# Kernel optimization log

Hardware: AMD Instinct MI355X
Metric: run time of the kernel (lower is better)

## Reference

```python
import jax, jax.numpy as jnp
import numpy as np

RANGES = {"measure": 256, "beat": 16, "position": 128, "duration": 128, "pitch": 256,
          "instrument": 129, "velocity": 128, "key_sign": 24, "time_sign": 48, "tempo": 49}
R_TOTAL = sum(RANGES.values())  # 1162
NUMERATORS = jnp.array([1, 2, 3, 4, 5, 6, 7, 8, 9, 10, 12, 16], dtype=jnp.int32)
TOT_NUM = 12
NEG = jnp.float32(-1e9)


def _prefix_gather(x, axis=1):
    # value at position i becomes the cumulative value at index min(i+1, S-1):
    # reproduces the tf mask `range(S) <= idx+1` (prefix up to i+1 inclusive).
    S = x.shape[axis]
    idx = jnp.minimum(jnp.arange(S) + 1, S - 1)
    return jnp.take(x, idx, axis=axis)


def _present_mask(song, dtype_id, feat, R):
    # occ[b,i,v] = True iff some token j<=i+1 has type dtype_id and song[b,j,feat]==v
    # (vectorized form of tensor_scatter_nd_max over a prefix, via one-hot + cummax)
    match = song[..., 0] == dtype_id                       # [B,S]
    onehot = (song[..., feat][..., None] == jnp.arange(R)) & match[..., None]
    cum = jax.lax.cummax(onehot.astype(jnp.int32), axis=1)
    return _prefix_gather(cum, 1).astype(bool)             # [B,S,R]


def _has_any(song, dtype_id):
    match = (song[..., 0] == dtype_id).astype(jnp.int32)
    return _prefix_gather(jax.lax.cummax(match, axis=1), 1).astype(bool)  # [B,S]


def _last_value(song, dtype_id, feat):
    # song[b, argmax_j(match*j) , feat] over the prefix j<=i+1; tf argmax of all
    # zeros returns 0, reproduced by where(match, j, 0) + cummax.
    match = song[..., 0] == dtype_id
    j = jnp.arange(song.shape[1])
    last_idx = _prefix_gather(jax.lax.cummax(jnp.where(match, j, 0), axis=1), 1)
    return jnp.take_along_axis(song[..., feat], last_idx, axis=1)  # [B,S]


def _forward(song, chosen_type, scores):
    B, S, _ = song.shape
    Rm, Rb = RANGES["measure"], RANGES["beat"]
    ar_m = jnp.arange(RANGES["measure"]); ar_b = jnp.arange(RANGES["beat"])
    ar_p = jnp.arange(RANGES["position"])
    ar_ks = jnp.arange(RANGES["key_sign"]); ar_ts = jnp.arange(RANGES["time_sign"])
    ar_tp = jnp.arange(RANGES["tempo"])
    t = chosen_type[..., None]  # [B,S,1]

    inst_present = _present_mask(song, 1, 6, RANGES["instrument"])  # [B,S,129]
    has_inst = inst_present.any(-1, keepdims=True)

    last_ks = _last_value(song, 4, 8);  oh_ks = last_ks[..., None] == ar_ks
    last_ts = _last_value(song, 5, 9);  oh_ts = last_ts[..., None] == ar_ts
    last_tp = _last_value(song, 6, 10); oh_tp = last_tp[..., None] == ar_tp
    has_ks = _has_any(song, 4)[..., None]
    has_ts = _has_any(song, 5)[..., None]

    # ---- chosen_type == 3 (note-like token) ----
    min_measure = song[..., 1]
    pred_m = jnp.argmax(scores[..., :Rm], axis=-1).astype(jnp.int32)
    c1 = pred_m == min_measure
    min_beat = jnp.where(c1, song[..., 2], 0)
    pred_b = jnp.argmax(scores[..., Rm:Rm + Rb], axis=-1).astype(jnp.int32)
    c2 = c1 & (pred_b == min_beat)
    min_pos = jnp.where(c2, song[..., 3], 0)
    max_beat = NUMERATORS[jnp.mod(last_ts, TOT_NUM)]  # get_max_beat_from_time_sign
    m3 = ar_m >= min_measure[..., None]
    b3 = (ar_b >= min_beat[..., None]) & (ar_b < max_beat[..., None])
    p3 = ar_p >= min_pos[..., None]

    # ---- chosen_type == 1 (instrument): forbid already-present instruments ----
    inst1 = jnp.where(has_inst, ~inst_present, True)

    # ---- chosen_type in 4..6 (key_sign / time_sign / tempo) ----
    min_m46 = jnp.where((song[..., 2] == 0) & (song[..., 3] == 0),
                        song[..., 1], song[..., 1] + 1)
    m46 = ar_m >= min_m46[..., None]
    ks4 = jnp.where(has_ks, ~oh_ks, True)
    ts5 = jnp.where(has_ts, ~oh_ts, True)
    tp6 = ~oh_tp

    is3 = t == 3
    measure_mask = jnp.where(is3, m3, jnp.where((t >= 4) & (t <= 6), m46, True))
    beat_mask = jnp.where(is3, b3, True)
    position_mask = jnp.where(is3, p3, True)
    duration_mask = jnp.ones((B, S, RANGES["duration"]), bool)
    pitch_mask = jnp.ones((B, S, RANGES["pitch"]), bool)
    instrument_mask = jnp.where(is3, inst_present, jnp.where(t == 1, inst1, True))
    velocity_mask = jnp.ones((B, S, RANGES["velocity"]), bool)
    key_sign_mask = jnp.where(is3, oh_ks, jnp.where(t == 4, ks4, True))
    time_sign_mask = jnp.where(is3, oh_ts, jnp.where(t == 5, ts5, True))
    tempo_mask = jnp.where(is3, oh_tp, jnp.where(t == 6, tp6, True))

    mask = jnp.concatenate([measure_mask, beat_mask, position_mask, duration_mask,
                            pitch_mask, instrument_mask, velocity_mask,
                            key_sign_mask, time_sign_mask, tempo_mask], axis=-1)
    return jnp.where(mask, scores, NEG)  # masked logits [B,S,R_TOTAL]


def setup_inputs() -> dict:
    key = jax.random.key(0)
    k_song, k_type, k_scores = jax.random.split(key, 3)
    B, S = 8, 2047  # SEQ_LEN-1 with SEQ_LEN=2048
    col_max = [8, RANGES["measure"], RANGES["beat"], RANGES["position"],
               RANGES["duration"], RANGES["pitch"], RANGES["instrument"],
               RANGES["velocity"], RANGES["key_sign"], RANGES["time_sign"],
               RANGES["tempo"]]
    kcols = jax.random.split(k_song, 11)
    song = jnp.stack([jax.random.randint(kcols[c], (B, S), 0, col_max[c],
                                         dtype=jnp.int32) for c in range(11)], axis=-1)
    chosen_type = jax.random.randint(k_type, (B, S), 0, 8, dtype=jnp.int32)
    scores = jax.random.normal(k_scores, (B, S, R_TOTAL), dtype=jnp.float32)
    return {"song": song, "chosen_type": chosen_type, "scores": scores}


def reference(song, chosen_type, scores):
    return _forward(song, chosen_type, scores)
```

## Files before the change

kernel.cpp:

```cpp
#include <hip/hip_runtime.h>
#include <cstdint>
#include <cstddef>

#define S_LEN 2047
#define BATCH 8
#define R_TOT 1162
#define NCHUNK 8
#define NEGV (-1e9f)

#define CARRY_OFF 393024

__device__ __constant__ int d_numerators[12] = {1, 2, 3, 4, 5, 6, 7, 8, 9, 10, 12, 16};

__global__ __launch_bounds__(256) void scan_local(const int* __restrict__ song,
                                                  unsigned* __restrict__ local) {
    const int b = blockIdx.x >> 3;
    const int c = blockIdx.x & 7;
    const int tid = threadIdx.x;
    const int j = c * 256 + tid;
    __shared__ unsigned lds_f[3][256];
    __shared__ unsigned lds_inst[5][256];
    const unsigned HAS = 1u << 16;
    const long base = (long)b * S_LEN;

    unsigned e_f[3] = {0, 0, 0};
    unsigned e_inst[5] = {0, 0, 0, 0, 0};
    if (j < S_LEN) {
        const int* rj = song + (base + j) * 11;
        const int type = rj[0];
        if (type == 4)      e_f[0] = HAS | (unsigned)rj[8];
        else if (type == 5) e_f[1] = HAS | (unsigned)rj[9];
        else if (type == 6) e_f[2] = HAS | (unsigned)rj[10];
        else if (type == 1) { const int v = rj[6]; e_inst[v >> 5] = 1u << (v & 31); }
    }
#pragma unroll
    for (int w = 0; w < 3; w++) lds_f[w][tid] = e_f[w];
#pragma unroll
    for (int w = 0; w < 5; w++) lds_inst[w][tid] = e_inst[w];
    __syncthreads();

    for (int off = 1; off < 256; off <<= 1) {
        unsigned p_f[3] = {0, 0, 0};
        unsigned p_inst[5] = {0, 0, 0, 0, 0};
        if (tid >= off) {
#pragma unroll
            for (int w = 0; w < 3; w++) p_f[w] = lds_f[w][tid - off];
#pragma unroll
            for (int w = 0; w < 5; w++) p_inst[w] = lds_inst[w][tid - off];
        }
        __syncthreads();
        if (tid >= off) {
#pragma unroll
            for (int w = 0; w < 3; w++) {
                if (!(e_f[w] & HAS)) e_f[w] = p_f[w];
                lds_f[w][tid] = e_f[w];
            }
#pragma unroll
            for (int w = 0; w < 5; w++) {
                e_inst[w] |= p_inst[w];
                lds_inst[w][tid] = e_inst[w];
            }
        }
        __syncthreads();
    }

    if (j < S_LEN) {
        const unsigned w0 =
            (e_f[0] & 0xFFu) | ((e_f[1] & 0xFFu) << 8) | ((e_f[2] & 0xFFu) << 16) |
            (((e_f[0] >> 16) & 1u) << 24) | (((e_f[1] >> 16) & 1u) << 25) |
            (((e_f[2] >> 16) & 1u) << 26);
        unsigned* sp = local + (size_t)(base + j) * 6;
        sp[0] = w0;
#pragma unroll
        for (int w = 0; w < 5; w++) sp[1 + w] = e_inst[w];
    }
}

__global__ __launch_bounds__(64) void scan_carry(const int* __restrict__ song,
                                                 const unsigned* __restrict__ local,
                                                 unsigned* __restrict__ carry) {
    const int b = threadIdx.x;
    if (b >= BATCH) return;
    const int* r0 = song + (size_t)b * S_LEN * 11;
    unsigned cks = (unsigned)r0[8], cts = (unsigned)r0[9], ctp = (unsigned)r0[10];
    unsigned chas = 0;
    unsigned cinst[5] = {0, 0, 0, 0, 0};
    for (int c = 0; c < NCHUNK; c++) {
        unsigned* cp = carry + ((size_t)b * NCHUNK + c) * 6;
        cp[0] = (cks & 0xFFu) | ((cts & 0xFFu) << 8) | ((ctp & 0xFFu) << 16) | (chas << 24);
#pragma unroll
        for (int w = 0; w < 5; w++) cp[1 + w] = cinst[w];
        const int pos = min((c + 1) * 256, S_LEN) - 1;
        const unsigned* lp = local + ((size_t)b * S_LEN + pos) * 6;
        const unsigned a0 = lp[0];
        if ((a0 >> 24) & 1u) cks = a0 & 0xFFu;
        if ((a0 >> 25) & 1u) cts = (a0 >> 8) & 0xFFu;
        if ((a0 >> 26) & 1u) ctp = (a0 >> 16) & 0xFFu;
        chas |= (a0 >> 24) & 7u;
#pragma unroll
        for (int w = 0; w < 5; w++) cinst[w] |= lp[1 + w];
    }
}

__global__ __launch_bounds__(256) void mask_kernel(const int* __restrict__ song,
                                                   const int* __restrict__ ctype,
                                                   const float* __restrict__ scores,
                                                   const unsigned* __restrict__ local,
                                                   const unsigned* __restrict__ carry,
                                                   float* __restrict__ out) {
    const int row = blockIdx.x;
    const int tid = threadIdx.x;
    const int b = row / S_LEN;
    const int i = row - b * S_LEN;

    __shared__ float s_val[128];
    __shared__ int   s_idx[128];
    __shared__ float sb_val[8];
    __shared__ int   sb_idx[8];
    __shared__ int   s_info[10];
    __shared__ int   f_info[17];

    const size_t rbase = (size_t)row * R_TOT;
    const float2* s2 = (const float2*)(scores + rbase);
    float2* o2 = (float2*)(out + rbase);

    const float2 r0 = s2[tid];
    const float2 r1 = s2[tid + 256];
    float2 r2 = make_float2(0.f, 0.f);
    if (tid < 69) r2 = s2[tid + 512];

    if (tid < 128) {
        const bool sec = (r0.y > r0.x);
        s_val[tid] = sec ? r0.y : r0.x;
        s_idx[tid] = 2 * tid + (sec ? 1 : 0);
    } else if (tid < 136) {
        const bool sec = (r0.y > r0.x);
        sb_val[tid - 128] = sec ? r0.y : r0.x;
        sb_idx[tid - 128] = (2 * tid - 256) + (sec ? 1 : 0);
    } else if (tid < 142) {
        const int w = tid - 136;
        const int e = min(i + 1, S_LEN - 1);
        const unsigned lw = local[((size_t)b * S_LEN + e) * 6 + w];
        const unsigned cw = carry[((size_t)b * NCHUNK + (e >> 8)) * 6 + w];
        unsigned v;
        if (w == 0) {
            const unsigned ks = ((lw >> 24) & 1u) ? (lw & 0xFFu) : (cw & 0xFFu);
            const unsigned ts = ((lw >> 25) & 1u) ? ((lw >> 8) & 0xFFu) : ((cw >> 8) & 0xFFu);
            const unsigned tp = ((lw >> 26) & 1u) ? ((lw >> 16) & 0xFFu) : ((cw >> 16) & 0xFFu);
            const unsigned hks = ((lw >> 24) | (cw >> 24)) & 1u;
            const unsigned hts = ((lw >> 25) | (cw >> 25)) & 1u;
            v = ks | (ts << 8) | (tp << 16) | (hks << 24) | (hts << 25);
        } else {
            v = lw | cw;
        }
        s_info[w] = (int)v;
    } else if (tid < 146) {
        const int* srow = song + (size_t)row * 11;
        if (tid == 142) s_info[6] = srow[1];
        if (tid == 143) s_info[7] = srow[2];
        if (tid == 144) s_info[8] = srow[3];
        if (tid == 145) s_info[9] = ctype[row];
    }
    __syncthreads();

    for (int s = 64; s > 0; s >>= 1) {
        if (tid < s) {
            if (s_val[tid + s] > s_val[tid]) {
                s_val[tid] = s_val[tid + s];
                s_idx[tid] = s_idx[tid + s];
            }
        }
        __syncthreads();
    }

    if (tid == 0) {
        const int pred_m = s_idx[0];
        float bv = sb_val[0];
        int pred_b = sb_idx[0];
#pragma unroll
        for (int q = 1; q < 8; q++) {
            if (sb_val[q] > bv) { bv = sb_val[q]; pred_b = sb_idx[q]; }
        }
        const unsigned pack = (unsigned)s_info[0];
        const int song1 = s_info[6], song2 = s_info[7], song3 = s_info[8];
        const int t = s_info[9];
        const bool c1 = (pred_m == song1);
        const int min_beat = c1 ? song2 : 0;
        const bool c2 = c1 && (pred_b == min_beat);
        const int min_pos = c2 ? song3 : 0;
        const int last_ks = pack & 0xFF;
        const int last_ts = (pack >> 8) & 0xFF;
        const int last_tp = (pack >> 16) & 0xFF;
        f_info[0] = t;
        f_info[1] = song1;
        f_info[2] = min_beat;
        f_info[3] = min_pos;
        f_info[4] = (song2 == 0 && song3 == 0) ? song1 : song1 + 1;
        f_info[5] = d_numerators[last_ts % 12];
        f_info[6] = last_ks;
        f_info[7] = last_ts;
        f_info[8] = last_tp;
        f_info[9]  = (int)((pack >> 24) & 1u);
        f_info[10] = (int)((pack >> 25) & 1u);
        const unsigned u = (unsigned)s_info[1] | (unsigned)s_info[2] | (unsigned)s_info[3] |
                           (unsigned)s_info[4] | (unsigned)s_info[5];
        f_info[11] = (u != 0u);
        f_info[12] = s_info[1]; f_info[13] = s_info[2]; f_info[14] = s_info[3];
        f_info[15] = s_info[4]; f_info[16] = s_info[5];
    }
    __syncthreads();

    const int t = f_info[0];
    const int min_measure = f_info[1], min_beat = f_info[2], min_pos = f_info[3];
    const int min_m46 = f_info[4], max_beat = f_info[5];
    const int last_ks = f_info[6], last_ts = f_info[7], last_tp = f_info[8];
    const bool has_ks = f_info[9] != 0, has_ts = f_info[10] != 0, has_inst = f_info[11] != 0;
    unsigned inst[5];
#pragma unroll
    for (int w = 0; w < 5; w++) inst[w] = (unsigned)f_info[12 + w];
    const bool is3 = (t == 3);
    const bool is46 = (t >= 4) && (t <= 6);

    auto maskf = [&](int col) -> bool {
        if (col < 256) {
            if (is3) return col >= min_measure;
            if (is46) return col >= min_m46;
            return true;
        } else if (col < 272) {
            if (!is3) return true;
            const int v = col - 256;
            return (v >= min_beat) && (v < max_beat);
        } else if (col < 400) {
            return is3 ? ((col - 272) >= min_pos) : true;
        } else if (col < 784) {
            return true;
        } else if (col < 913) {
            const int v = col - 784;
            const bool pres = ((inst[v >> 5] >> (v & 31)) & 1u) != 0u;
            if (is3) return pres;
            if (t == 1) return has_inst ? !pres : true;
            return true;
        } else if (col < 1041) {
            return true;
        } else if (col < 1065) {
            const int v = col - 1041;
            if (is3) return v == last_ks;
            if (t == 4) return has_ks ? (v != last_ks) : true;
            return true;
        } else if (col < 1113) {
            const int v = col - 1065;
            if (is3) return v == last_ts;
            if (t == 5) return has_ts ? (v != last_ts) : true;
            return true;
        } else {
            const int v = col - 1113;
            if (is3) return v == last_tp;
            if (t == 6) return v != last_tp;
            return true;
        }
    };

    float2 w;
    int c = 2 * tid;
    w.x = maskf(c)     ? r0.x : NEGV;
    w.y = maskf(c + 1) ? r0.y : NEGV;
    o2[tid] = w;

    c = 512 + 2 * tid;
    w.x = maskf(c)     ? r1.x : NEGV;
    w.y = maskf(c + 1) ? r1.y : NEGV;
    o2[tid + 256] = w;

    if (tid < 69) {
        c = 1024 + 2 * tid;
        w.x = maskf(c)     ? r2.x : NEGV;
        w.y = maskf(c + 1) ? r2.y : NEGV;
        o2[tid + 512] = w;
    }
}

extern "C" void kernel_launch(void* const* d_in, const int* in_sizes, int n_in,
                              void* d_out, int out_size, void* d_ws, size_t ws_size,
                              hipStream_t stream) {
    const int* song = (const int*)d_in[0];
    const int* ctype = (const int*)d_in[1];
    const float* scores = (const float*)d_in[2];
    float* out = (float*)d_out;
    unsigned* local = (unsigned*)d_ws;
    unsigned* carry = (unsigned*)((char*)d_ws + CARRY_OFF);

    scan_local<<<BATCH * NCHUNK, 256, 0, stream>>>(song, local);
    scan_carry<<<1, 64, 0, stream>>>(song, local, carry);
    mask_kernel<<<BATCH * S_LEN, 256, 0, stream>>>(song, ctype, scores, local, carry, out);
}
```

Measured before the change: 154.2 us.

## Split mask kernel into param pass and float4 row-pair apply pass

Splits the per-row mask kernel in two. A param kernel computes each row's argmax and prefix state and writes it to a workspace array. An apply kernel then processes two rows per block with float4 loads and stores, which the even 2*R_TOT pair size allows. The aim is wider, aligned memory traffic in the bandwidth-bound apply pass. In exchange it adds a kernel launch and reads the first 512 scores of every row a second time in the param pass.

```diff
diff --git a/kernel.cpp b/kernel.cpp
--- a/kernel.cpp
+++ b/kernel.cpp
@@ -9,6 +9,8 @@
 #define NEGV (-1e9f)
 
 #define CARRY_OFF 393024
+#define PARAM_OFF 394560
+#define PSTRIDE 18
 
 __device__ __constant__ int d_numerators[12] = {1, 2, 3, 4, 5, 6, 7, 8, 9, 10, 12, 16};
 
@@ -102,12 +104,12 @@
     }
 }
 
-__global__ __launch_bounds__(256) void mask_kernel(const int* __restrict__ song,
-                                                   const int* __restrict__ ctype,
-                                                   const float* __restrict__ scores,
-                                                   const unsigned* __restrict__ local,
-                                                   const unsigned* __restrict__ carry,
-                                                   float* __restrict__ out) {
+__global__ __launch_bounds__(256) void param_kernel(const int* __restrict__ song,
+                                                    const int* __restrict__ ctype,
+                                                    const float* __restrict__ scores,
+                                                    const unsigned* __restrict__ local,
+                                                    const unsigned* __restrict__ carry,
+                                                    int* __restrict__ params) {
     const int row = blockIdx.x;
     const int tid = threadIdx.x;
     const int b = row / S_LEN;
@@ -118,16 +120,11 @@
     __shared__ float sb_val[8];
     __shared__ int   sb_idx[8];
     __shared__ int   s_info[10];
-    __shared__ int   f_info[17];
 
     const size_t rbase = (size_t)row * R_TOT;
     const float2* s2 = (const float2*)(scores + rbase);
-    float2* o2 = (float2*)(out + rbase);
 
     const float2 r0 = s2[tid];
-    const float2 r1 = s2[tid + 256];
-    float2 r2 = make_float2(0.f, 0.f);
-    if (tid < 69) r2 = s2[tid + 512];
 
     if (tid < 128) {
         const bool sec = (r0.y > r0.x);
@@ -188,94 +185,144 @@
         const int min_beat = c1 ? song2 : 0;
         const bool c2 = c1 && (pred_b == min_beat);
         const int min_pos = c2 ? song3 : 0;
-        const int last_ks = pack & 0xFF;
-        const int last_ts = (pack >> 8) & 0xFF;
-        const int last_tp = (pack >> 16) & 0xFF;
-        f_info[0] = t;
-        f_info[1] = song1;
-        f_info[2] = min_beat;
-        f_info[3] = min_pos;
-        f_info[4] = (song2 == 0 && song3 == 0) ? song1 : song1 + 1;
-        f_info[5] = d_numerators[last_ts % 12];
-        f_info[6] = last_ks;
-        f_info[7] = last_ts;
-        f_info[8] = last_tp;
-        f_info[9]  = (int)((pack >> 24) & 1u);
-        f_info[10] = (int)((pack >> 25) & 1u);
+        const int last_ks = (int)(pack & 0xFFu);
+        const int last_ts = (int)((pack >> 8) & 0xFFu);
+        const int last_tp = (int)((pack >> 16) & 0xFFu);
         const unsigned u = (unsigned)s_info[1] | (unsigned)s_info[2] | (unsigned)s_info[3] |
                            (unsigned)s_info[4] | (unsigned)s_info[5];
-        f_info[11] = (u != 0u);
-        f_info[12] = s_info[1]; f_info[13] = s_info[2]; f_info[14] = s_info[3];
-        f_info[15] = s_info[4]; f_info[16] = s_info[5];
-    }
-    __syncthreads();
-
-    const int t = f_info[0];
-    const int min_measure = f_info[1], min_beat = f_info[2], min_pos = f_info[3];
-    const int min_m46 = f_info[4], max_beat = f_info[5];
-    const int last_ks = f_info[6], last_ts = f_info[7], last_tp = f_info[8];
-    const bool has_ks = f_info[9] != 0, has_ts = f_info[10] != 0, has_inst = f_info[11] != 0;
+        int* pp = params + (size_t)row * PSTRIDE;
+        pp[0] = t;
+        pp[1] = song1;
+        pp[2] = min_beat;
+        pp[3] = min_pos;
+        pp[4] = (song2 == 0 && song3 == 0) ? song1 : song1 + 1;
+        pp[5] = d_numerators[last_ts % 12];
+        pp[6] = last_ks;
+        pp[7] = last_ts;
+        pp[8] = last_tp;
+        pp[9]  = (int)((pack >> 24) & 1u);
+        pp[10] = (int)((pack >> 25) & 1u);
+        pp[11] = (u != 0u);
+        pp[12] = s_info[1]; pp[13] = s_info[2]; pp[14] = s_info[3];
+        pp[15] = s_info[4]; pp[16] = s_info[5];
+    }
+}
+
+struct P {
+    int t, min_measure, min_beat, min_pos, min_m46, max_beat;
+    int last_ks, last_ts, last_tp;
+    int has_ks, has_ts, has_inst;
     unsigned inst[5];
-#pragma unroll
-    for (int w = 0; w < 5; w++) inst[w] = (unsigned)f_info[12 + w];
-    const bool is3 = (t == 3);
-    const bool is46 = (t >= 4) && (t <= 6);
-
-    auto maskf = [&](int col) -> bool {
-        if (col < 256) {
-            if (is3) return col >= min_measure;
-            if (is46) return col >= min_m46;
-            return true;
-        } else if (col < 272) {
-            if (!is3) return true;
-            const int v = col - 256;
-            return (v >= min_beat) && (v < max_beat);
-        } else if (col < 400) {
-            return is3 ? ((col - 272) >= min_pos) : true;
-        } else if (col < 784) {
-            return true;
-        } else if (col < 913) {
-            const int v = col - 784;
-            const bool pres = ((inst[v >> 5] >> (v & 31)) & 1u) != 0u;
-            if (is3) return pres;
-            if (t == 1) return has_inst ? !pres : true;
-            return true;
-        } else if (col < 1041) {
-            return true;
-        } else if (col < 1065) {
-            const int v = col - 1041;
-            if (is3) return v == last_ks;
-            if (t == 4) return has_ks ? (v != last_ks) : true;
-            return true;
-        } else if (col < 1113) {
-            const int v = col - 1065;
-            if (is3) return v == last_ts;
-            if (t == 5) return has_ts ? (v != last_ts) : true;
-            return true;
+};
+
+__device__ __forceinline__ void load_params(const int* __restrict__ pp, P& p) {
+    p.t = pp[0]; p.min_measure = pp[1]; p.min_beat = pp[2]; p.min_pos = pp[3];
+    p.min_m46 = pp[4]; p.max_beat = pp[5];
+    p.last_ks = pp[6]; p.last_ts = pp[7]; p.last_tp = pp[8];
+    p.has_ks = pp[9]; p.has_ts = pp[10]; p.has_inst = pp[11];
+#pragma unroll
+    for (int w = 0; w < 5; w++) p.inst[w] = (unsigned)pp[12 + w];
+}
+
+__device__ __forceinline__ bool maskf(const P& p, int col) {
+    const bool is3 = (p.t == 3);
+    const bool is46 = (p.t >= 4) && (p.t <= 6);
+    if (col < 256) {
+        if (is3) return col >= p.min_measure;
+        if (is46) return col >= p.min_m46;
+        return true;
+    } else if (col < 272) {
+        if (!is3) return true;
+        const int v = col - 256;
+        return (v >= p.min_beat) && (v < p.max_beat);
+    } else if (col < 400) {
+        return is3 ? ((col - 272) >= p.min_pos) : true;
+    } else if (col < 784) {
+        return true;
+    } else if (col < 913) {
+        const int v = col - 784;
+        const bool pres = ((p.inst[v >> 5] >> (v & 31)) & 1u) != 0u;
+        if (is3) return pres;
+        if (p.t == 1) return p.has_inst ? !pres : true;
+        return true;
+    } else if (col < 1041) {
+        return true;
+    } else if (col < 1065) {
+        const int v = col - 1041;
+        if (is3) return v == p.last_ks;
+        if (p.t == 4) return p.has_ks ? (v != p.last_ks) : true;
+        return true;
+    } else if (col < 1113) {
+        const int v = col - 1065;
+        if (is3) return v == p.last_ts;
+        if (p.t == 5) return p.has_ts ? (v != p.last_ts) : true;
+        return true;
+    } else {
+        const int v = col - 1113;
+        if (is3) return v == p.last_tp;
+        if (p.t == 6) return v != p.last_tp;
+        return true;
+    }
+}
+
+__global__ __launch_bounds__(256) void apply2_kernel(const float* __restrict__ scores,
+                                                     const int* __restrict__ params,
+                                                     float* __restrict__ out) {
+    const int pair = blockIdx.x;
+    const int tid = threadIdx.x;
+    const size_t base = (size_t)pair * (2 * R_TOT);
+    const float4* s4 = (const float4*)(scores + base);
+    float4* o4 = (float4*)(out + base);
+
+    const float4 r0 = s4[tid];
+    const float4 r1 = s4[tid + 256];
+    float4 r2 = make_float4(0.f, 0.f, 0.f, 0.f);
+    if (tid < 69) r2 = s4[tid + 512];
+
+    P A, B;
+    load_params(params + (size_t)(2 * pair) * PSTRIDE, A);
+    load_params(params + (size_t)(2 * pair + 1) * PSTRIDE, B);
+
+    {
+        const int c = 4 * tid;
+        float4 w;
+        w.x = maskf(A, c)     ? r0.x : NEGV;
+        w.y = maskf(A, c + 1) ? r0.y : NEGV;
+        w.z = maskf(A, c + 2) ? r0.z : NEGV;
+        w.w = maskf(A, c + 3) ? r0.w : NEGV;
+        o4[tid] = w;
+    }
+    {
+        const int f = tid + 256;
+        float4 w;
+        if (f < 290) {
+            const int c = 4 * f;
+            w.x = maskf(A, c)     ? r1.x : NEGV;
+            w.y = maskf(A, c + 1) ? r1.y : NEGV;
+            w.z = maskf(A, c + 2) ? r1.z : NEGV;
+            w.w = maskf(A, c + 3) ? r1.w : NEGV;
+        } else if (f == 290) {
+            w.x = maskf(A, 1160) ? r1.x : NEGV;
+            w.y = maskf(A, 1161) ? r1.y : NEGV;
+            w.z = maskf(B, 0)    ? r1.z : NEGV;
+            w.w = maskf(B, 1)    ? r1.w : NEGV;
         } else {
-            const int v = col - 1113;
-            if (is3) return v == last_tp;
-            if (t == 6) return v != last_tp;
-            return true;
-        }
-    };
-
-    float2 w;
-    int c = 2 * tid;
-    w.x = maskf(c)     ? r0.x : NEGV;
-    w.y = maskf(c + 1) ? r0.y : NEGV;
-    o2[tid] = w;
-
-    c = 512 + 2 * tid;
-    w.x = maskf(c)     ? r1.x : NEGV;
-    w.y = maskf(c + 1) ? r1.y : NEGV;
-    o2[tid + 256] = w;
-
+            const int c = 4 * f - R_TOT;
+            w.x = maskf(B, c)     ? r1.x : NEGV;
+            w.y = maskf(B, c + 1) ? r1.y : NEGV;
+            w.z = maskf(B, c + 2) ? r1.z : NEGV;
+            w.w = maskf(B, c + 3) ? r1.w : NEGV;
+        }
+        o4[tid + 256] = w;
+    }
     if (tid < 69) {
-        c = 1024 + 2 * tid;
-        w.x = maskf(c)     ? r2.x : NEGV;
-        w.y = maskf(c + 1) ? r2.y : NEGV;
-        o2[tid + 512] = w;
+        const int c = 4 * (tid + 512) - R_TOT;
+        float4 w;
+        w.x = maskf(B, c)     ? r2.x : NEGV;
+        w.y = maskf(B, c + 1) ? r2.y : NEGV;
+        w.z = maskf(B, c + 2) ? r2.z : NEGV;
+        w.w = maskf(B, c + 3) ? r2.w : NEGV;
+        o4[tid + 512] = w;
     }
 }
 
@@ -288,8 +335,10 @@
     float* out = (float*)d_out;
     unsigned* local = (unsigned*)d_ws;
     unsigned* carry = (unsigned*)((char*)d_ws + CARRY_OFF);
+    int* params = (int*)((char*)d_ws + PARAM_OFF);
 
     scan_local<<<BATCH * NCHUNK, 256, 0, stream>>>(song, local);
     scan_carry<<<1, 64, 0, stream>>>(song, local, carry);
-    mask_kernel<<<BATCH * S_LEN, 256, 0, stream>>>(song, ctype, scores, local, carry, out);
-}
+    param_kernel<<<BATCH * S_LEN, 256, 0, stream>>>(song, ctype, scores, local, carry, params);
+    apply2_kernel<<<(BATCH * S_LEN) / 2, 256, 0, stream>>>(scores, params, out);
+}
```

Result: slower. 185.4 us (+20.2%).
